# Kernel tuning notes

Measured on AMD Instinct MI355X. Metric: run time of the kernel, lower is better.

The kernel has to match this reference:

```python
import jax, jax.numpy as jnp
import numpy as np

# Block structure (mirrors init_kwargs)
K = 8            # number of blocks
BLK = 1024       # per-block in/out width
TOTAL = K * BLK  # total_dim = 8192
INPUT_IDX = [(i * BLK, (i + 1) * BLK) for i in range(K)]
OUTPUT_IDX = [(((i + 1) % K) * BLK, ((i + 1) % K + 1) * BLK) for i in range(K)]
BATCH = 4096


def setup_inputs() -> dict:
    key = jax.random.key(0)
    k1, k2, k3, k4 = jax.random.split(key, 4)
    x = jax.random.normal(k1, (BATCH, TOTAL), dtype=jnp.float32)
    v = jax.random.normal(k2, (BATCH, TOTAL), dtype=jnp.float32)
    # Per-block Linear params; nn.Linear default init ~ U(-1/sqrt(in), 1/sqrt(in))
    bound = 1.0 / np.sqrt(BLK)
    W = jax.random.uniform(k3, (K, BLK, BLK), dtype=jnp.float32, minval=-bound, maxval=bound)  # [K, out, in]
    b = jax.random.uniform(k4, (K, BLK), dtype=jnp.float32, minval=-bound, maxval=bound)
    return {"x": x, "v": v, "W": W, "b": b}


def reference(x, v, W, b):
    # hidden = act(v)
    hidden = jnp.tanh(v)
    # All input blocks are a uniform partition -> batch the K small GEMMs as one grouped contraction.
    h = hidden.reshape(BATCH, K, BLK)                      # [B, K, in]
    y = jnp.einsum("bki,koi->bko", h, W) + b               # [B, K, out]
    # Scatter-accumulate each block output into its padded position, plus residual x.
    result = x
    for i, (o0, o1) in enumerate(OUTPUT_IDX):
        result = result.at[:, o0:o1].add(y[:, i])
    return result
```

## Files before the change

kernel.cpp:

```cpp
#include <hip/hip_runtime.h>
#include <hip/hip_bf16.h>
#include <stdint.h>

#define BATCH 4096
#define KGRP  8
#define BLK   1024
#define TOTAL 8192

typedef __attribute__((ext_vector_type(8))) short short8;
typedef __attribute__((ext_vector_type(4))) float f32x4;


__device__ __forceinline__ unsigned short f2bf(float f) {
    union { float f; uint32_t u; } c; c.f = f;
    uint32_t u = c.u;
    u += 0x7fffu + ((u >> 16) & 1u);
    return (unsigned short)(u >> 16);
}

__device__ __forceinline__ float fast_tanh(float x) {
    float e = __expf(2.0f * x);
    return 1.0f - 2.0f / (e + 1.0f);
}


__global__ void k_tanh_cast(const float4* __restrict__ v, ushort4* __restrict__ H) {
    const int n4 = BATCH * TOTAL / 4;
    int i = blockIdx.x * blockDim.x + threadIdx.x;
    const int stride = gridDim.x * blockDim.x;
    for (; i < n4; i += stride) {
        float4 f = v[i];
        ushort4 o;
        o.x = f2bf(fast_tanh(f.x));
        o.y = f2bf(fast_tanh(f.y));
        o.z = f2bf(fast_tanh(f.z));
        o.w = f2bf(fast_tanh(f.w));
        H[i] = o;
    }
}

__global__ void k_wcast(const float4* __restrict__ W, ushort4* __restrict__ Wb) {
    const int n4 = KGRP * BLK * BLK / 4;
    int i = blockIdx.x * blockDim.x + threadIdx.x;
    const int stride = gridDim.x * blockDim.x;
    for (; i < n4; i += stride) {
        float4 f = W[i];
        ushort4 o;
        o.x = f2bf(f.x); o.y = f2bf(f.y); o.z = f2bf(f.z); o.w = f2bf(f.w);
        Wb[i] = o;
    }
}


__global__ __launch_bounds__(512, 2)
void k_gemm(const unsigned short* __restrict__ H, const unsigned short* __restrict__ Wb,
            const float* __restrict__ x, const float* __restrict__ bias,
            float* __restrict__ out) {
    __shared__ __attribute__((aligned(1024))) char lds[131072];

    const int bid   = blockIdx.x;
    const int g     = bid & 7;
    const int slot  = bid >> 3;
    const int mtile = slot >> 2;
    const int ntile = slot & 3;

    const int tid  = threadIdx.x;
    const int lane = tid & 63;
    const int w    = tid >> 6;
    const int wr   = w >> 2;
    const int wc   = w & 3;

    const uint32_t flip  = (uint32_t)(((lane >> 2) & 1) << 5);
    const uint32_t kcol  = ((uint32_t)((lane >> 4) * 16)) ^ flip;
    const uint32_t aBase = (uint32_t)(wr * 128 + (lane & 15)) * 128u + kcol;
    const uint32_t bBase = 32768u + (uint32_t)(wc * 64 + (lane & 15)) * 128u + kcol;

    const int sRow = tid >> 3;
    const int sCol = ((tid & 7) * 8) ^ (((tid >> 5) & 1) << 4);
    const unsigned short* Asrc0 = H  + ((size_t)(mtile * 256) + sRow) * TOTAL + (size_t)g * BLK + sCol;
    const unsigned short* Bsrc0 = Wb + ((size_t)g * BLK * BLK) + ((size_t)(ntile * 256) + sRow) * BLK + sCol;
    const uint32_t ldsStageBase = (uint32_t)(w << 10);

    auto stageA = [&](int kt, uint32_t bufb) {
#pragma unroll
        for (int c = 0; c < 4; ++c)
            __builtin_amdgcn_global_load_lds(
                (const __attribute__((address_space(1))) uint32_t*)(Asrc0 + (size_t)(c * 64) * TOTAL + kt * 64),
                (__attribute__((address_space(3))) uint32_t*)(lds + bufb + c * 8192 + ldsStageBase),
                16, 0, 0);
    };
    auto stageB = [&](int kt, uint32_t bufb) {
#pragma unroll
        for (int c = 0; c < 4; ++c)
            __builtin_amdgcn_global_load_lds(
                (const __attribute__((address_space(1))) uint32_t*)(Bsrc0 + (size_t)(c * 64) * BLK + kt * 64),
                (__attribute__((address_space(3))) uint32_t*)(lds + bufb + 32768u + c * 8192 + ldsStageBase),
                16, 0, 0);
    };

    f32x4 acc[8][4];
#pragma unroll
    for (int m = 0; m < 8; ++m)
#pragma unroll
        for (int n = 0; n < 4; ++n) acc[m][n] = (f32x4){0.f, 0.f, 0.f, 0.f};

    stageA(0, 0u);
    stageB(0, 0u);
    asm volatile("s_waitcnt vmcnt(0)" ::: "memory");
    __builtin_amdgcn_s_barrier();
    __builtin_amdgcn_sched_barrier(0);

    uint32_t cur = 0;
    for (int kt = 0; kt < 16; ++kt) {
        const uint32_t bufb = cur << 16;
        const uint32_t nbuf = bufb ^ 65536u;
        const char* Lb = lds + bufb;
        const bool st = (kt < 15);

        short8 bfr[4][2];
        short8 am[2][2];

#pragma unroll
        for (int n = 0; n < 4; ++n)
#pragma unroll
            for (int ks = 0; ks < 2; ++ks)
                bfr[n][ks] = *(const short8*)(Lb + bBase + n * 2048 + ks * 64);
#pragma unroll
        for (int i = 0; i < 2; ++i)
#pragma unroll
            for (int ks = 0; ks < 2; ++ks)
                am[i][ks] = *(const short8*)(Lb + aBase + (0 + i) * 2048 + ks * 64);
        if (st) stageA(kt + 1, nbuf);
        __builtin_amdgcn_s_barrier();
        __builtin_amdgcn_s_setprio(1);
#pragma unroll
        for (int i = 0; i < 2; ++i)
#pragma unroll
            for (int n = 0; n < 4; ++n)
#pragma unroll
                for (int ks = 0; ks < 2; ++ks)
                    acc[0 + i][n] = __builtin_amdgcn_mfma_f32_16x16x32_bf16(am[i][ks], bfr[n][ks], acc[0 + i][n], 0, 0, 0);
        __builtin_amdgcn_s_setprio(0);
        __builtin_amdgcn_s_barrier();

#pragma unroll
        for (int i = 0; i < 2; ++i)
#pragma unroll
            for (int ks = 0; ks < 2; ++ks)
                am[i][ks] = *(const short8*)(Lb + aBase + (2 + i) * 2048 + ks * 64);
        if (st) stageB(kt + 1, nbuf);
        __builtin_amdgcn_s_barrier();
        __builtin_amdgcn_s_setprio(1);
#pragma unroll
        for (int i = 0; i < 2; ++i)
#pragma unroll
            for (int n = 0; n < 4; ++n)
#pragma unroll
                for (int ks = 0; ks < 2; ++ks)
                    acc[2 + i][n] = __builtin_amdgcn_mfma_f32_16x16x32_bf16(am[i][ks], bfr[n][ks], acc[2 + i][n], 0, 0, 0);
        __builtin_amdgcn_s_setprio(0);
        __builtin_amdgcn_s_barrier();

#pragma unroll
        for (int i = 0; i < 2; ++i)
#pragma unroll
            for (int ks = 0; ks < 2; ++ks)
                am[i][ks] = *(const short8*)(Lb + aBase + (4 + i) * 2048 + ks * 64);
        __builtin_amdgcn_s_barrier();
        __builtin_amdgcn_s_setprio(1);
#pragma unroll
        for (int i = 0; i < 2; ++i)
#pragma unroll
            for (int n = 0; n < 4; ++n)
#pragma unroll
                for (int ks = 0; ks < 2; ++ks)
                    acc[4 + i][n] = __builtin_amdgcn_mfma_f32_16x16x32_bf16(am[i][ks], bfr[n][ks], acc[4 + i][n], 0, 0, 0);
        __builtin_amdgcn_s_setprio(0);
        __builtin_amdgcn_s_barrier();

#pragma unroll
        for (int i = 0; i < 2; ++i)
#pragma unroll
            for (int ks = 0; ks < 2; ++ks)
                am[i][ks] = *(const short8*)(Lb + aBase + (6 + i) * 2048 + ks * 64);
        __builtin_amdgcn_s_barrier();
        __builtin_amdgcn_s_setprio(1);
#pragma unroll
        for (int i = 0; i < 2; ++i)
#pragma unroll
            for (int n = 0; n < 4; ++n)
#pragma unroll
                for (int ks = 0; ks < 2; ++ks)
                    acc[6 + i][n] = __builtin_amdgcn_mfma_f32_16x16x32_bf16(am[i][ks], bfr[n][ks], acc[6 + i][n], 0, 0, 0);
        __builtin_amdgcn_s_setprio(0);

        asm volatile("s_waitcnt vmcnt(0)" ::: "memory");
        __builtin_amdgcn_s_barrier();
        __builtin_amdgcn_sched_barrier(0);
        cur ^= 1u;
    }

    const int gout = (g + 1) & 7;
    const int row0 = mtile * 256 + wr * 128 + ((lane >> 4) << 2);
    const int colL = ntile * 256 + wc * 64 + (lane & 15);
    float bv[4];
#pragma unroll
    for (int n = 0; n < 4; ++n) bv[n] = bias[g * BLK + colL + n * 16];
#pragma unroll
    for (int m = 0; m < 8; ++m) {
#pragma unroll
        for (int j = 0; j < 4; ++j) {
            const int row = row0 + m * 16 + j;
            const size_t base = (size_t)row * TOTAL + (size_t)gout * BLK;
#pragma unroll
            for (int n = 0; n < 4; ++n) {
                const size_t idx = base + colL + n * 16;
                out[idx] = x[idx] + bv[n] + acc[m][n][j];
            }
        }
    }
}


__global__ void k_naive(const float* __restrict__ x, const float* __restrict__ v,
                        const float* __restrict__ W, const float* __restrict__ b,
                        float* __restrict__ out) {
    __shared__ float hv[BLK];
    const int bid = blockIdx.x;
    const int quarter = bid & 3;
    const int g = (bid >> 2) & 7;
    const int row = bid >> 5;
    for (int i = threadIdx.x; i < BLK; i += 256)
        hv[i] = tanhf(v[(size_t)row * TOTAL + g * BLK + i]);
    __syncthreads();
    const int o = quarter * 256 + threadIdx.x;
    const float* wrow = W + ((size_t)g * BLK + o) * BLK;
    float s = 0.f;
    for (int i = 0; i < BLK; ++i) s += hv[i] * wrow[i];
    const size_t oi = (size_t)row * TOTAL + (size_t)((g + 1) & 7) * BLK + o;
    out[oi] = x[oi] + b[g * BLK + o] + s;
}


extern "C" void kernel_launch(void* const* d_in, const int* in_sizes, int n_in,
                              void* d_out, int out_size, void* d_ws, size_t ws_size,
                              hipStream_t stream) {
    const float* x = (const float*)d_in[0];
    const float* v = (const float*)d_in[1];
    const float* W = (const float*)d_in[2];
    const float* b = (const float*)d_in[3];
    float* out = (float*)d_out;

    const size_t needH = (size_t)BATCH * TOTAL * sizeof(unsigned short);
    const size_t needW = (size_t)KGRP * BLK * BLK * sizeof(unsigned short);

    if (ws_size >= needH + needW) {
        unsigned short* H  = (unsigned short*)d_ws;
        unsigned short* Wb = (unsigned short*)((char*)d_ws + needH);
        k_tanh_cast<<<2048, 256, 0, stream>>>((const float4*)v, (ushort4*)H);
        k_wcast<<<1024, 256, 0, stream>>>((const float4*)W, (ushort4*)Wb);
        k_gemm<<<512, 512, 0, stream>>>(H, Wb, x, b, out);
    } else {
        k_naive<<<BATCH * KGRP * 4, 256, 0, stream>>>(x, v, W, b, out);
    }
}
```

Before: 161.0 us.

## Split global-to-LDS staging into halves with partial vmcnt waits and full XOR swizzle

Splits each A/B tile prefetch into two halves issued across the four compute phases, and replaces the full vmcnt(0) drain with partial waits (vmcnt(2)/vmcnt(4)) so loads stay in flight across barriers. The last k-tile is peeled into an epilogue with no prefetch. The LDS layout also moves from a single-bit flip to a full 3-bit XOR swizzle on the 16-byte column, applied both when staging and when reading fragments, to cut bank conflicts. The risk is that the partial-wait counts or the half ordering are wrong, which would let waves read LDS data that has not arrived yet.

Result: faster. 155.5 us (-3.4%).

```diff
diff --git a/kernel.cpp b/kernel.cpp
--- a/kernel.cpp
+++ b/kernel.cpp
@@ -9,6 +9,9 @@
 
 typedef __attribute__((ext_vector_type(8))) short short8;
 typedef __attribute__((ext_vector_type(4))) float f32x4;
+
+#define AS1 __attribute__((address_space(1)))
+#define AS3 __attribute__((address_space(3)))
 
 
 __device__ __forceinline__ unsigned short f2bf(float f) {
@@ -70,32 +73,36 @@
     const int wr   = w >> 2;
     const int wc   = w & 3;
 
-    const uint32_t flip  = (uint32_t)(((lane >> 2) & 1) << 5);
-    const uint32_t kcol  = ((uint32_t)((lane >> 4) * 16)) ^ flip;
-    const uint32_t aBase = (uint32_t)(wr * 128 + (lane & 15)) * 128u + kcol;
-    const uint32_t bBase = 32768u + (uint32_t)(wc * 64 + (lane & 15)) * 128u + kcol;
+    uint32_t kc[2];
+#pragma unroll
+    for (int ks = 0; ks < 2; ++ks)
+        kc[ks] = (uint32_t)((ks * 64 + ((lane >> 4) << 4)) ^ ((lane & 7) << 4));
+    const uint32_t aRow = (uint32_t)(wr * 128 + (lane & 15)) * 128u;
+    const uint32_t bRow = 32768u + (uint32_t)(wc * 64 + (lane & 15)) * 128u;
 
     const int sRow = tid >> 3;
-    const int sCol = ((tid & 7) * 8) ^ (((tid >> 5) & 1) << 4);
+    const int sCol = (((lane & 7) ^ ((lane >> 3) & 7)) << 3);
     const unsigned short* Asrc0 = H  + ((size_t)(mtile * 256) + sRow) * TOTAL + (size_t)g * BLK + sCol;
     const unsigned short* Bsrc0 = Wb + ((size_t)g * BLK * BLK) + ((size_t)(ntile * 256) + sRow) * BLK + sCol;
     const uint32_t ldsStageBase = (uint32_t)(w << 10);
 
-    auto stageA = [&](int kt, uint32_t bufb) {
-#pragma unroll
-        for (int c = 0; c < 4; ++c)
+    auto stageA2 = [&](int kt, uint32_t bufb, int half) {
+#pragma unroll
+        for (int h = 0; h < 2; ++h) {
+            const int c = half + h * 2;
             __builtin_amdgcn_global_load_lds(
-                (const __attribute__((address_space(1))) uint32_t*)(Asrc0 + (size_t)(c * 64) * TOTAL + kt * 64),
-                (__attribute__((address_space(3))) uint32_t*)(lds + bufb + c * 8192 + ldsStageBase),
-                16, 0, 0);
+                (const AS1 uint32_t*)(Asrc0 + (size_t)(c * 64) * TOTAL + kt * 64),
+                (AS3 uint32_t*)(lds + bufb + c * 8192 + ldsStageBase), 16, 0, 0);
+        }
     };
-    auto stageB = [&](int kt, uint32_t bufb) {
-#pragma unroll
-        for (int c = 0; c < 4; ++c)
+    auto stageB2 = [&](int kt, uint32_t bufb, int half) {
+#pragma unroll
+        for (int h = 0; h < 2; ++h) {
+            const int c = half * 2 + h;
             __builtin_amdgcn_global_load_lds(
-                (const __attribute__((address_space(1))) uint32_t*)(Bsrc0 + (size_t)(c * 64) * BLK + kt * 64),
-                (__attribute__((address_space(3))) uint32_t*)(lds + bufb + 32768u + c * 8192 + ldsStageBase),
-                16, 0, 0);
+                (const AS1 uint32_t*)(Bsrc0 + (size_t)(c * 64) * BLK + kt * 64),
+                (AS3 uint32_t*)(lds + bufb + 32768u + c * 8192 + ldsStageBase), 16, 0, 0);
+        }
     };
 
     f32x4 acc[8][4];
@@ -104,18 +111,19 @@
 #pragma unroll
         for (int n = 0; n < 4; ++n) acc[m][n] = (f32x4){0.f, 0.f, 0.f, 0.f};
 
-    stageA(0, 0u);
-    stageB(0, 0u);
-    asm volatile("s_waitcnt vmcnt(0)" ::: "memory");
+    stageA2(0, 0u, 0);
+    stageB2(0, 0u, 0);
+    stageB2(0, 0u, 1);
+    stageA2(0, 0u, 1);
+    asm volatile("s_waitcnt vmcnt(2)" ::: "memory");
     __builtin_amdgcn_s_barrier();
     __builtin_amdgcn_sched_barrier(0);
 
     uint32_t cur = 0;
-    for (int kt = 0; kt < 16; ++kt) {
+    for (int kt = 0; kt < 15; ++kt) {
         const uint32_t bufb = cur << 16;
         const uint32_t nbuf = bufb ^ 65536u;
         const char* Lb = lds + bufb;
-        const bool st = (kt < 15);
 
         short8 bfr[4][2];
         short8 am[2][2];
@@ -124,13 +132,13 @@
         for (int n = 0; n < 4; ++n)
 #pragma unroll
             for (int ks = 0; ks < 2; ++ks)
-                bfr[n][ks] = *(const short8*)(Lb + bBase + n * 2048 + ks * 64);
-#pragma unroll
-        for (int i = 0; i < 2; ++i)
-#pragma unroll
-            for (int ks = 0; ks < 2; ++ks)
-                am[i][ks] = *(const short8*)(Lb + aBase + (0 + i) * 2048 + ks * 64);
-        if (st) stageA(kt + 1, nbuf);
+                bfr[n][ks] = *(const short8*)(Lb + bRow + n * 2048 + kc[ks]);
+#pragma unroll
+        for (int i = 0; i < 2; ++i)
+#pragma unroll
+            for (int ks = 0; ks < 2; ++ks)
+                am[i][ks] = *(const short8*)(Lb + aRow + (0 + i) * 2048 + kc[ks]);
+        stageA2(kt + 1, nbuf, 0);
         __builtin_amdgcn_s_barrier();
         __builtin_amdgcn_s_setprio(1);
 #pragma unroll
@@ -147,8 +155,8 @@
         for (int i = 0; i < 2; ++i)
 #pragma unroll
             for (int ks = 0; ks < 2; ++ks)
-                am[i][ks] = *(const short8*)(Lb + aBase + (2 + i) * 2048 + ks * 64);
-        if (st) stageB(kt + 1, nbuf);
+                am[i][ks] = *(const short8*)(Lb + aRow + (2 + i) * 2048 + kc[ks]);
+        stageB2(kt + 1, nbuf, 0);
         __builtin_amdgcn_s_barrier();
         __builtin_amdgcn_s_setprio(1);
 #pragma unroll
@@ -159,13 +167,15 @@
                 for (int ks = 0; ks < 2; ++ks)
                     acc[2 + i][n] = __builtin_amdgcn_mfma_f32_16x16x32_bf16(am[i][ks], bfr[n][ks], acc[2 + i][n], 0, 0, 0);
         __builtin_amdgcn_s_setprio(0);
-        __builtin_amdgcn_s_barrier();
-
-#pragma unroll
-        for (int i = 0; i < 2; ++i)
-#pragma unroll
-            for (int ks = 0; ks < 2; ++ks)
-                am[i][ks] = *(const short8*)(Lb + aBase + (4 + i) * 2048 + ks * 64);
+        asm volatile("s_waitcnt vmcnt(4)" ::: "memory");
+        __builtin_amdgcn_s_barrier();
+
+#pragma unroll
+        for (int i = 0; i < 2; ++i)
+#pragma unroll
+            for (int ks = 0; ks < 2; ++ks)
+                am[i][ks] = *(const short8*)(Lb + aRow + (4 + i) * 2048 + kc[ks]);
+        stageB2(kt + 1, nbuf, 1);
         __builtin_amdgcn_s_barrier();
         __builtin_amdgcn_s_setprio(1);
 #pragma unroll
@@ -182,7 +192,8 @@
         for (int i = 0; i < 2; ++i)
 #pragma unroll
             for (int ks = 0; ks < 2; ++ks)
-                am[i][ks] = *(const short8*)(Lb + aBase + (6 + i) * 2048 + ks * 64);
+                am[i][ks] = *(const short8*)(Lb + aRow + (6 + i) * 2048 + kc[ks]);
+        stageA2(kt + 1, nbuf, 1);
         __builtin_amdgcn_s_barrier();
         __builtin_amdgcn_s_setprio(1);
 #pragma unroll
@@ -193,11 +204,89 @@
                 for (int ks = 0; ks < 2; ++ks)
                     acc[6 + i][n] = __builtin_amdgcn_mfma_f32_16x16x32_bf16(am[i][ks], bfr[n][ks], acc[6 + i][n], 0, 0, 0);
         __builtin_amdgcn_s_setprio(0);
-
-        asm volatile("s_waitcnt vmcnt(0)" ::: "memory");
+        asm volatile("s_waitcnt vmcnt(2)" ::: "memory");
         __builtin_amdgcn_s_barrier();
         __builtin_amdgcn_sched_barrier(0);
         cur ^= 1u;
+    }
+
+    {
+        const char* Lb = lds + (cur << 16);
+        short8 bfr[4][2];
+        short8 am[2][2];
+
+#pragma unroll
+        for (int n = 0; n < 4; ++n)
+#pragma unroll
+            for (int ks = 0; ks < 2; ++ks)
+                bfr[n][ks] = *(const short8*)(Lb + bRow + n * 2048 + kc[ks]);
+#pragma unroll
+        for (int i = 0; i < 2; ++i)
+#pragma unroll
+            for (int ks = 0; ks < 2; ++ks)
+                am[i][ks] = *(const short8*)(Lb + aRow + (0 + i) * 2048 + kc[ks]);
+        __builtin_amdgcn_s_barrier();
+        __builtin_amdgcn_s_setprio(1);
+#pragma unroll
+        for (int i = 0; i < 2; ++i)
+#pragma unroll
+            for (int n = 0; n < 4; ++n)
+#pragma unroll
+                for (int ks = 0; ks < 2; ++ks)
+                    acc[0 + i][n] = __builtin_amdgcn_mfma_f32_16x16x32_bf16(am[i][ks], bfr[n][ks], acc[0 + i][n], 0, 0, 0);
+        __builtin_amdgcn_s_setprio(0);
+        __builtin_amdgcn_s_barrier();
+
+#pragma unroll
+        for (int i = 0; i < 2; ++i)
+#pragma unroll
+            for (int ks = 0; ks < 2; ++ks)
+                am[i][ks] = *(const short8*)(Lb + aRow + (2 + i) * 2048 + kc[ks]);
+        __builtin_amdgcn_s_barrier();
+        __builtin_amdgcn_s_setprio(1);
+#pragma unroll
+        for (int i = 0; i < 2; ++i)
+#pragma unroll
+            for (int n = 0; n < 4; ++n)
+#pragma unroll
+                for (int ks = 0; ks < 2; ++ks)
+                    acc[2 + i][n] = __builtin_amdgcn_mfma_f32_16x16x32_bf16(am[i][ks], bfr[n][ks], acc[2 + i][n], 0, 0, 0);
+        __builtin_amdgcn_s_setprio(0);
+        asm volatile("s_waitcnt vmcnt(0)" ::: "memory");
+        __builtin_amdgcn_s_barrier();
+
+#pragma unroll
+        for (int i = 0; i < 2; ++i)
+#pragma unroll
+            for (int ks = 0; ks < 2; ++ks)
+                am[i][ks] = *(const short8*)(Lb + aRow + (4 + i) * 2048 + kc[ks]);
+        __builtin_amdgcn_s_barrier();
+        __builtin_amdgcn_s_setprio(1);
+#pragma unroll
+        for (int i = 0; i < 2; ++i)
+#pragma unroll
+            for (int n = 0; n < 4; ++n)
+#pragma unroll
+                for (int ks = 0; ks < 2; ++ks)
+                    acc[4 + i][n] = __builtin_amdgcn_mfma_f32_16x16x32_bf16(am[i][ks], bfr[n][ks], acc[4 + i][n], 0, 0, 0);
+        __builtin_amdgcn_s_setprio(0);
+        __builtin_amdgcn_s_barrier();
+
+#pragma unroll
+        for (int i = 0; i < 2; ++i)
+#pragma unroll
+            for (int ks = 0; ks < 2; ++ks)
+                am[i][ks] = *(const short8*)(Lb + aRow + (6 + i) * 2048 + kc[ks]);
+        __builtin_amdgcn_s_barrier();
+        __builtin_amdgcn_s_setprio(1);
+#pragma unroll
+        for (int i = 0; i < 2; ++i)
+#pragma unroll
+            for (int n = 0; n < 4; ++n)
+#pragma unroll
+                for (int ks = 0; ks < 2; ++ks)
+                    acc[6 + i][n] = __builtin_amdgcn_mfma_f32_16x16x32_bf16(am[i][ks], bfr[n][ks], acc[6 + i][n], 0, 0, 0);
+        __builtin_amdgcn_s_setprio(0);
     }
 
     const int gout = (g + 1) & 7;
```

## Deepen GEMM load pipeline with split staging, full XOR swizzle, fused prep kernels

Applied to the files above, without the earlier changes.

Restructures the GEMM main loop so global-to-LDS loads run further ahead. B and half of A for tile kt+2 are issued into the current buffer after its data has been consumed, and partial vmcnt waits replace the full drain at the end of each iteration. The LDS layout switches to an 8-way XOR swizzle across all eight 16-byte columns to cut bank conflicts. The tanh-cast and weight-cast kernels are merged into one launch. The tighter wait counts and extra barriers make the schedule fragile, and any miscounted vmcnt would silently read stale LDS.

After: 153.8 us. 4.5% less time.

```diff
diff --git a/kernel.cpp b/kernel.cpp
--- a/kernel.cpp
+++ b/kernel.cpp
@@ -9,6 +9,9 @@
 
 typedef __attribute__((ext_vector_type(8))) short short8;
 typedef __attribute__((ext_vector_type(4))) float f32x4;
+
+#define AS1 __attribute__((address_space(1)))
+#define AS3 __attribute__((address_space(3)))
 
 
 __device__ __forceinline__ unsigned short f2bf(float f) {
@@ -24,39 +27,134 @@
 }
 
 
-__global__ void k_tanh_cast(const float4* __restrict__ v, ushort4* __restrict__ H) {
-    const int n4 = BATCH * TOTAL / 4;
-    int i = blockIdx.x * blockDim.x + threadIdx.x;
-    const int stride = gridDim.x * blockDim.x;
-    for (; i < n4; i += stride) {
-        float4 f = v[i];
-        ushort4 o;
-        o.x = f2bf(fast_tanh(f.x));
-        o.y = f2bf(fast_tanh(f.y));
-        o.z = f2bf(fast_tanh(f.z));
-        o.w = f2bf(fast_tanh(f.w));
-        H[i] = o;
-    }
-}
-
-__global__ void k_wcast(const float4* __restrict__ W, ushort4* __restrict__ Wb) {
-    const int n4 = KGRP * BLK * BLK / 4;
-    int i = blockIdx.x * blockDim.x + threadIdx.x;
-    const int stride = gridDim.x * blockDim.x;
-    for (; i < n4; i += stride) {
-        float4 f = W[i];
-        ushort4 o;
-        o.x = f2bf(f.x); o.y = f2bf(f.y); o.z = f2bf(f.z); o.w = f2bf(f.w);
-        Wb[i] = o;
-    }
-}
-
+__global__ void k_prep(const float4* __restrict__ v, ushort4* __restrict__ H,
+                       const float4* __restrict__ W, ushort4* __restrict__ Wb) {
+    const int b = blockIdx.x;
+    if (b < 2048) {
+        const int n4 = BATCH * TOTAL / 4;
+        for (int i = b * 256 + threadIdx.x; i < n4; i += 2048 * 256) {
+            float4 f = v[i];
+            ushort4 o;
+            o.x = f2bf(fast_tanh(f.x)); o.y = f2bf(fast_tanh(f.y));
+            o.z = f2bf(fast_tanh(f.z)); o.w = f2bf(fast_tanh(f.w));
+            H[i] = o;
+        }
+    } else {
+        const int n4 = KGRP * BLK * BLK / 4;
+        for (int i = (b - 2048) * 256 + threadIdx.x; i < n4; i += 512 * 256) {
+            float4 f = W[i];
+            ushort4 o;
+            o.x = f2bf(f.x); o.y = f2bf(f.y); o.z = f2bf(f.z); o.w = f2bf(f.w);
+            Wb[i] = o;
+        }
+    }
+}
+
+
+__device__ __forceinline__ void stage_a(const unsigned short* Asrc0, char* ldsp,
+                                        uint32_t bufb, uint32_t sb, int kt, int half) {
+#pragma unroll
+    for (int h = 0; h < 2; ++h) {
+        const int c = half + h * 2;
+        __builtin_amdgcn_global_load_lds(
+            (const AS1 uint32_t*)(Asrc0 + (size_t)(c * 64) * TOTAL + kt * 64),
+            (AS3 uint32_t*)(ldsp + bufb + c * 8192 + sb), 16, 0, 0);
+    }
+}
+
+__device__ __forceinline__ void stage_b(const unsigned short* Bsrc0, char* ldsp,
+                                        uint32_t bufb, uint32_t sb, int kt) {
+#pragma unroll
+    for (int c = 0; c < 4; ++c) {
+        __builtin_amdgcn_global_load_lds(
+            (const AS1 uint32_t*)(Bsrc0 + (size_t)(c * 64) * BLK + kt * 64),
+            (AS3 uint32_t*)(ldsp + bufb + 32768u + c * 8192 + sb), 16, 0, 0);
+    }
+}
+
+template<int N> __device__ __forceinline__ void waitvm() {
+    if constexpr (N == 0)       asm volatile("s_waitcnt vmcnt(0)" ::: "memory");
+    else if constexpr (N == 2)  asm volatile("s_waitcnt vmcnt(2)" ::: "memory");
+    else if constexpr (N == 8)  asm volatile("s_waitcnt vmcnt(8)" ::: "memory");
+    else if constexpr (N == 12) asm volatile("s_waitcnt vmcnt(12)" ::: "memory");
+}
+
+template<int M0>
+__device__ __forceinline__ void mfma_phase(const short8 am[2][2], const short8 bfr[4][2],
+                                           f32x4 (*acc)[4]) {
+    __builtin_amdgcn_s_barrier();
+    __builtin_amdgcn_s_setprio(1);
+#pragma unroll
+    for (int i = 0; i < 2; ++i)
+#pragma unroll
+        for (int n = 0; n < 4; ++n)
+#pragma unroll
+            for (int ks = 0; ks < 2; ++ks)
+                acc[M0 + i][n] = __builtin_amdgcn_mfma_f32_16x16x32_bf16(am[i][ks], bfr[n][ks], acc[M0 + i][n], 0, 0, 0);
+    __builtin_amdgcn_s_setprio(0);
+}
+
+template<bool SA13, bool SB, bool SA02, int W1, int W3>
+__device__ __forceinline__ void tile_body(int kt, uint32_t bufb, char* ldsp,
+                                          uint32_t aRow, uint32_t bRow, const uint32_t* kc,
+                                          f32x4 (*acc)[4],
+                                          const unsigned short* Asrc0, const unsigned short* Bsrc0,
+                                          uint32_t sb) {
+    const char* Lb = ldsp + bufb;
+    short8 bfr[4][2], am[2][2];
+
+#pragma unroll
+    for (int n = 0; n < 4; ++n)
+#pragma unroll
+        for (int ks = 0; ks < 2; ++ks)
+            bfr[n][ks] = *(const short8*)(Lb + bRow + n * 2048 + kc[ks]);
+#pragma unroll
+    for (int i = 0; i < 2; ++i)
+#pragma unroll
+        for (int ks = 0; ks < 2; ++ks)
+            am[i][ks] = *(const short8*)(Lb + aRow + i * 2048 + kc[ks]);
+    if constexpr (SA13) stage_a(Asrc0, ldsp, bufb ^ 65536u, sb, kt + 1, 1);
+    mfma_phase<0>(am, bfr, acc);
+    __builtin_amdgcn_s_barrier();
+
+#pragma unroll
+    for (int i = 0; i < 2; ++i)
+#pragma unroll
+        for (int ks = 0; ks < 2; ++ks)
+            am[i][ks] = *(const short8*)(Lb + aRow + (2 + i) * 2048 + kc[ks]);
+    if constexpr (SB) stage_b(Bsrc0, ldsp, bufb, sb, kt + 2);
+    mfma_phase<2>(am, bfr, acc);
+    waitvm<W1>();
+    __builtin_amdgcn_s_barrier();
+
+#pragma unroll
+    for (int i = 0; i < 2; ++i)
+#pragma unroll
+        for (int ks = 0; ks < 2; ++ks)
+            am[i][ks] = *(const short8*)(Lb + aRow + (4 + i) * 2048 + kc[ks]);
+    if constexpr (SA02) stage_a(Asrc0, ldsp, bufb, sb, kt + 2, 0);
+    mfma_phase<4>(am, bfr, acc);
+    __builtin_amdgcn_s_barrier();
+
+#pragma unroll
+    for (int i = 0; i < 2; ++i)
+#pragma unroll
+        for (int ks = 0; ks < 2; ++ks)
+            am[i][ks] = *(const short8*)(Lb + aRow + (6 + i) * 2048 + kc[ks]);
+    mfma_phase<6>(am, bfr, acc);
+    if constexpr (W3 >= 0) {
+        waitvm<W3>();
+        __builtin_amdgcn_s_barrier();
+        __builtin_amdgcn_sched_barrier(0);
+    }
+}
 
 __global__ __launch_bounds__(512, 2)
 void k_gemm(const unsigned short* __restrict__ H, const unsigned short* __restrict__ Wb,
             const float* __restrict__ x, const float* __restrict__ bias,
             float* __restrict__ out) {
     __shared__ __attribute__((aligned(1024))) char lds[131072];
+    char* ldsp = lds;
 
     const int bid   = blockIdx.x;
     const int g     = bid & 7;
@@ -70,33 +168,18 @@
     const int wr   = w >> 2;
     const int wc   = w & 3;
 
-    const uint32_t flip  = (uint32_t)(((lane >> 2) & 1) << 5);
-    const uint32_t kcol  = ((uint32_t)((lane >> 4) * 16)) ^ flip;
-    const uint32_t aBase = (uint32_t)(wr * 128 + (lane & 15)) * 128u + kcol;
-    const uint32_t bBase = 32768u + (uint32_t)(wc * 64 + (lane & 15)) * 128u + kcol;
+    uint32_t kc[2];
+#pragma unroll
+    for (int ks = 0; ks < 2; ++ks)
+        kc[ks] = (uint32_t)((ks * 64 + ((lane >> 4) << 4)) ^ ((lane & 7) << 4));
+    const uint32_t aRow = (uint32_t)(wr * 128 + (lane & 15)) * 128u;
+    const uint32_t bRow = 32768u + (uint32_t)(wc * 64 + (lane & 15)) * 128u;
 
     const int sRow = tid >> 3;
-    const int sCol = ((tid & 7) * 8) ^ (((tid >> 5) & 1) << 4);
+    const int sCol = (((lane & 7) ^ ((lane >> 3) & 7)) << 3);
     const unsigned short* Asrc0 = H  + ((size_t)(mtile * 256) + sRow) * TOTAL + (size_t)g * BLK + sCol;
     const unsigned short* Bsrc0 = Wb + ((size_t)g * BLK * BLK) + ((size_t)(ntile * 256) + sRow) * BLK + sCol;
-    const uint32_t ldsStageBase = (uint32_t)(w << 10);
-
-    auto stageA = [&](int kt, uint32_t bufb) {
-#pragma unroll
-        for (int c = 0; c < 4; ++c)
-            __builtin_amdgcn_global_load_lds(
-                (const __attribute__((address_space(1))) uint32_t*)(Asrc0 + (size_t)(c * 64) * TOTAL + kt * 64),
-                (__attribute__((address_space(3))) uint32_t*)(lds + bufb + c * 8192 + ldsStageBase),
-                16, 0, 0);
-    };
-    auto stageB = [&](int kt, uint32_t bufb) {
-#pragma unroll
-        for (int c = 0; c < 4; ++c)
-            __builtin_amdgcn_global_load_lds(
-                (const __attribute__((address_space(1))) uint32_t*)(Bsrc0 + (size_t)(c * 64) * BLK + kt * 64),
-                (__attribute__((address_space(3))) uint32_t*)(lds + bufb + 32768u + c * 8192 + ldsStageBase),
-                16, 0, 0);
-    };
+    const uint32_t sb = (uint32_t)(w << 10);
 
     f32x4 acc[8][4];
 #pragma unroll
@@ -104,101 +187,24 @@
 #pragma unroll
         for (int n = 0; n < 4; ++n) acc[m][n] = (f32x4){0.f, 0.f, 0.f, 0.f};
 
-    stageA(0, 0u);
-    stageB(0, 0u);
-    asm volatile("s_waitcnt vmcnt(0)" ::: "memory");
+    stage_b(Bsrc0, ldsp, 0u, sb, 0);
+    stage_a(Asrc0, ldsp, 0u, sb, 0, 0);
+    stage_a(Asrc0, ldsp, 0u, sb, 0, 1);
+    stage_b(Bsrc0, ldsp, 65536u, sb, 1);
+    stage_a(Asrc0, ldsp, 65536u, sb, 1, 0);
+    waitvm<8>();
     __builtin_amdgcn_s_barrier();
     __builtin_amdgcn_sched_barrier(0);
 
     uint32_t cur = 0;
-    for (int kt = 0; kt < 16; ++kt) {
-        const uint32_t bufb = cur << 16;
-        const uint32_t nbuf = bufb ^ 65536u;
-        const char* Lb = lds + bufb;
-        const bool st = (kt < 15);
-
-        short8 bfr[4][2];
-        short8 am[2][2];
-
-#pragma unroll
-        for (int n = 0; n < 4; ++n)
-#pragma unroll
-            for (int ks = 0; ks < 2; ++ks)
-                bfr[n][ks] = *(const short8*)(Lb + bBase + n * 2048 + ks * 64);
-#pragma unroll
-        for (int i = 0; i < 2; ++i)
-#pragma unroll
-            for (int ks = 0; ks < 2; ++ks)
-                am[i][ks] = *(const short8*)(Lb + aBase + (0 + i) * 2048 + ks * 64);
-        if (st) stageA(kt + 1, nbuf);
-        __builtin_amdgcn_s_barrier();
-        __builtin_amdgcn_s_setprio(1);
-#pragma unroll
-        for (int i = 0; i < 2; ++i)
-#pragma unroll
-            for (int n = 0; n < 4; ++n)
-#pragma unroll
-                for (int ks = 0; ks < 2; ++ks)
-                    acc[0 + i][n] = __builtin_amdgcn_mfma_f32_16x16x32_bf16(am[i][ks], bfr[n][ks], acc[0 + i][n], 0, 0, 0);
-        __builtin_amdgcn_s_setprio(0);
-        __builtin_amdgcn_s_barrier();
-
-#pragma unroll
-        for (int i = 0; i < 2; ++i)
-#pragma unroll
-            for (int ks = 0; ks < 2; ++ks)
-                am[i][ks] = *(const short8*)(Lb + aBase + (2 + i) * 2048 + ks * 64);
-        if (st) stageB(kt + 1, nbuf);
-        __builtin_amdgcn_s_barrier();
-        __builtin_amdgcn_s_setprio(1);
-#pragma unroll
-        for (int i = 0; i < 2; ++i)
-#pragma unroll
-            for (int n = 0; n < 4; ++n)
-#pragma unroll
-                for (int ks = 0; ks < 2; ++ks)
-                    acc[2 + i][n] = __builtin_amdgcn_mfma_f32_16x16x32_bf16(am[i][ks], bfr[n][ks], acc[2 + i][n], 0, 0, 0);
-        __builtin_amdgcn_s_setprio(0);
-        __builtin_amdgcn_s_barrier();
-
-#pragma unroll
-        for (int i = 0; i < 2; ++i)
-#pragma unroll
-            for (int ks = 0; ks < 2; ++ks)
-                am[i][ks] = *(const short8*)(Lb + aBase + (4 + i) * 2048 + ks * 64);
-        __builtin_amdgcn_s_barrier();
-        __builtin_amdgcn_s_setprio(1);
-#pragma unroll
-        for (int i = 0; i < 2; ++i)
-#pragma unroll
-            for (int n = 0; n < 4; ++n)
-#pragma unroll
-                for (int ks = 0; ks < 2; ++ks)
-                    acc[4 + i][n] = __builtin_amdgcn_mfma_f32_16x16x32_bf16(am[i][ks], bfr[n][ks], acc[4 + i][n], 0, 0, 0);
-        __builtin_amdgcn_s_setprio(0);
-        __builtin_amdgcn_s_barrier();
-
-#pragma unroll
-        for (int i = 0; i < 2; ++i)
-#pragma unroll
-            for (int ks = 0; ks < 2; ++ks)
-                am[i][ks] = *(const short8*)(Lb + aBase + (6 + i) * 2048 + ks * 64);
-        __builtin_amdgcn_s_barrier();
-        __builtin_amdgcn_s_setprio(1);
-#pragma unroll
-        for (int i = 0; i < 2; ++i)
-#pragma unroll
-            for (int n = 0; n < 4; ++n)
-#pragma unroll
-                for (int ks = 0; ks < 2; ++ks)
-                    acc[6 + i][n] = __builtin_amdgcn_mfma_f32_16x16x32_bf16(am[i][ks], bfr[n][ks], acc[6 + i][n], 0, 0, 0);
-        __builtin_amdgcn_s_setprio(0);
-
-        asm volatile("s_waitcnt vmcnt(0)" ::: "memory");
-        __builtin_amdgcn_s_barrier();
-        __builtin_amdgcn_sched_barrier(0);
+#pragma unroll 1
+    for (int kt = 0; kt < 14; ++kt) {
+        tile_body<true, true, true, 12, 8>(kt, cur << 16, ldsp, aRow, bRow, kc, acc, Asrc0, Bsrc0, sb);
         cur ^= 1u;
     }
+    tile_body<true, false, false, 8, 2>(14, cur << 16, ldsp, aRow, bRow, kc, acc, Asrc0, Bsrc0, sb);
+    cur ^= 1u;
+    tile_body<false, false, false, 0, -1>(15, cur << 16, ldsp, aRow, bRow, kc, acc, Asrc0, Bsrc0, sb);
 
     const int gout = (g + 1) & 7;
     const int row0 = mtile * 256 + wr * 128 + ((lane >> 4) << 2);
@@ -257,8 +263,8 @@
     if (ws_size >= needH + needW) {
         unsigned short* H  = (unsigned short*)d_ws;
         unsigned short* Wb = (unsigned short*)((char*)d_ws + needH);
-        k_tanh_cast<<<2048, 256, 0, stream>>>((const float4*)v, (ushort4*)H);
-        k_wcast<<<1024, 256, 0, stream>>>((const float4*)W, (ushort4*)Wb);
+        k_prep<<<2560, 256, 0, stream>>>((const float4*)v, (ushort4*)H,
+                                         (const float4*)W, (ushort4*)Wb);
         k_gemm<<<512, 512, 0, stream>>>(H, Wb, x, b, out);
     } else {
         k_naive<<<BATCH * KGRP * 4, 256, 0, stream>>>(x, v, W, b, out);
```
